# Optimization experiments

Measured on AMD Instinct MI355X. Metric: run time of the kernel, lower is better.

## Reference

```python
import jax, jax.numpy as jnp
import numpy as np

NUM_EXPERTS = 32
TOP_K = 8
HIDDEN = 1536
INTER = 512


def setup_inputs() -> dict:
    key = jax.random.key(0)
    k1, k2, k3, k4 = jax.random.split(key, 4)
    hidden_states = jax.random.normal(k1, (4, 2048, HIDDEN), dtype=jnp.float32)
    # gate (router) weight: [E, H] as in nn.Linear(hidden, num_experts)
    gate_w = jax.random.normal(k2, (NUM_EXPERTS, HIDDEN), dtype=jnp.float32) * 0.02
    # fused gate+up projection per expert: [E, 2*I, H] (first I rows = gate/silu path)
    w13 = jax.random.normal(k3, (NUM_EXPERTS, 2 * INTER, HIDDEN), dtype=jnp.float32) * 0.02
    # down projection per expert: [E, H, I]
    w2 = jax.random.normal(k4, (NUM_EXPERTS, HIDDEN, INTER), dtype=jnp.float32) * 0.02
    return {"hidden_states": hidden_states, "gate_w": gate_w, "w13": w13, "w2": w2}


def _moe_forward(x, gate_w, w13, w2):
    orig_shape = x.shape
    x = x.reshape(-1, HIDDEN)            # [T, H]
    T = x.shape[0]

    # Router: softmax over all experts, then top-k, then renormalize.
    router_logits = x @ gate_w.T          # [T, E]
    probs = jax.nn.softmax(router_logits, axis=-1)
    topk_w, topk_idx = jax.lax.top_k(probs, TOP_K)        # [T, K]
    topk_w = topk_w / jnp.sum(topk_w, axis=-1, keepdims=True)

    # Scatter top-k weights into a dense [T, E] combine matrix (zeros elsewhere).
    expert_w = jnp.zeros((T, NUM_EXPERTS), dtype=x.dtype)
    expert_w = expert_w.at[jnp.arange(T)[:, None], topk_idx].add(topk_w)
    expert_w_eT = expert_w.T              # [E, T]

    def body(acc, ew):
        we, w13_e, w2_e = ew              # [T], [2I, H], [H, I]
        gu = x @ w13_e.T                  # [T, 2I]
        g, u = gu[:, :INTER], gu[:, INTER:]
        y = (jax.nn.silu(g) * u) @ w2_e.T  # [T, H]
        return acc + we[:, None] * y, None

    out, _ = jax.lax.scan(body, jnp.zeros_like(x), (expert_w_eT, w13, w2))
    return out.reshape(orig_shape)


def reference(hidden_states, gate_w, w13, w2):
    return _moe_forward(hidden_states, gate_w, w13, w2)
```

## Files before the change

### kernel.cpp

```cpp
#include <hip/hip_runtime.h>
#include <hip/hip_bf16.h>
#include <math.h>

#define NUM_EXPERTS 32
#define TOP_K 8
#define HIDDEN 1536
#define INTER 512

typedef __bf16 bf16_t;
typedef __bf16 bf16x8 __attribute__((ext_vector_type(8)));
typedef __bf16 bf16x4 __attribute__((ext_vector_type(4)));
typedef float f32x4 __attribute__((ext_vector_type(4)));

#define M_COUNTS    0
#define M_OFFSETS   32
#define M_CURSORS   96
#define M_NUMTILES  128
#define M_TILE_E    256
#define M_TILE_M0   1024
#define M_TILE_ROWS 2048
#define META_BYTES  16384

__device__ __forceinline__ void gld16(void* lds, const void* gsrc) {
  __builtin_amdgcn_global_load_lds(
      (const __attribute__((address_space(1))) void*)gsrc,
      (__attribute__((address_space(3))) void*)lds, 16, 0, 0);
}

__global__ __launch_bounds__(256) void k_cvt(
    const float* __restrict__ src, bf16_t* __restrict__ dst)
{
  size_t i = ((size_t)blockIdx.x * 256 + threadIdx.x) * 4;
  f32x4 v = *(const f32x4*)(src + i);
  bf16x4 o;
  o[0] = (bf16_t)v[0]; o[1] = (bf16_t)v[1]; o[2] = (bf16_t)v[2]; o[3] = (bf16_t)v[3];
  *(bf16x4*)(dst + i) = o;
}

__global__ __launch_bounds__(256) void k_tgw(
    const float* __restrict__ gw, float* __restrict__ gwT4)
{
  int tid = blockIdx.x * 256 + threadIdx.x;
  int e = tid / HIDDEN, k = tid % HIDDEN;
  gwT4[(k >> 2) * 128 + (e << 2) + (k & 3)] = gw[tid];
}

__global__ __launch_bounds__(64) void k_router(
    const float* __restrict__ x, const float* __restrict__ gwT4,
    int* __restrict__ meta, int* __restrict__ topk_idx, float* __restrict__ topk_w,
    bf16_t* __restrict__ x16)
{
  int t = blockIdx.x;
  int lane = threadIdx.x;
  int e = lane & 31, part = lane >> 5;
  const float* xrow = x + (size_t)t * HIDDEN;
  const f32x4* xr = (const f32x4*)(xrow + part * 768);
  const f32x4* gr = (const f32x4*)(gwT4 + part * 192 * 128 + e * 4);
  float s = 0.f;
#pragma unroll 4
  for (int i = 0; i < 192; ++i) {
    f32x4 xv = xr[i];
    f32x4 gv = gr[i * 32];
    s += xv[0] * gv[0] + xv[1] * gv[1] + xv[2] * gv[2] + xv[3] * gv[3];
  }
  s += __shfl_xor(s, 32);

  {
    const f32x4* xv4 = (const f32x4*)(xrow + lane * 24);
    bf16_t* xo = x16 + (size_t)t * HIDDEN + lane * 24;
#pragma unroll
    for (int i = 0; i < 6; ++i) {
      f32x4 v = xv4[i];
      bf16x4 o;
      o[0] = (bf16_t)v[0]; o[1] = (bf16_t)v[1]; o[2] = (bf16_t)v[2]; o[3] = (bf16_t)v[3];
      *(bf16x4*)(xo + i * 4) = o;
    }
  }

  float logit = s, rem = s;
  float m0 = 0.f, wsum = 0.f, my_l = 0.f;
  int my_e = 0;
#pragma unroll
  for (int k = 0; k < TOP_K; ++k) {
    float mx = rem;
#pragma unroll
    for (int off = 32; off >= 1; off >>= 1) mx = fmaxf(mx, __shfl_xor(mx, off));
    unsigned long long bal = __ballot(rem == mx);
    int src = __ffsll(bal) - 1;
    int ex = src & 31;
    float lv = __shfl(logit, ex);
    if (k == 0) m0 = mx;
    wsum += __expf(lv - m0);
    if (lane == k) { my_e = ex; my_l = lv; }
    if ((lane & 31) == ex) rem = -1e30f;
  }
  if (lane < TOP_K) {
    topk_idx[t * TOP_K + lane] = my_e;
    topk_w[t * TOP_K + lane] = __expf(my_l - m0) / wsum;
    atomicAdd(&meta[M_COUNTS + my_e], 1);
  }
}

__global__ void k_scan(int* __restrict__ meta)
{
  if (threadIdx.x != 0 || blockIdx.x != 0) return;
  int off = 0, nt = 0;
  for (int e = 0; e < NUM_EXPERTS; ++e) {
    int n = meta[M_COUNTS + e];
    meta[M_OFFSETS + e] = off;
    meta[M_CURSORS + e] = off;
    int tn = (n + 127) >> 7;
    for (int i = 0; i < tn; ++i) {
      meta[M_TILE_E + nt] = e;
      meta[M_TILE_M0 + nt] = off + i * 128;
      meta[M_TILE_ROWS + nt] = min(128, n - i * 128);
      ++nt;
    }
    off += n;
  }
  meta[M_OFFSETS + NUM_EXPERTS] = off;
  meta[M_NUMTILES] = nt;
}

__global__ __launch_bounds__(256) void k_scatter(
    const int* __restrict__ topk_idx, const float* __restrict__ topk_w,
    int* __restrict__ meta, int* __restrict__ pair_token, float* __restrict__ pair_weight)
{
  int i = blockIdx.x * 256 + threadIdx.x;
  int e = topk_idx[i];
  int pos = atomicAdd(&meta[M_CURSORS + e], 1);
  pair_token[pos] = i >> 3;
  pair_weight[pos] = topk_w[i];
}

__global__ __launch_bounds__(256, 2) void k_gemm1(
    const bf16_t* __restrict__ x, const bf16_t* __restrict__ w13,
    const int* __restrict__ meta, const int* __restrict__ pair_token,
    bf16_t* __restrict__ act)
{
  int bid = blockIdx.x;
  int xcd = bid & 7, r2 = bid >> 3;
  int nb = r2 & 3, tile = xcd + 8 * (r2 >> 2);
  if (tile >= meta[M_NUMTILES]) return;
  int e    = meta[M_TILE_E + tile];
  int m0   = meta[M_TILE_M0 + tile];
  int rows = meta[M_TILE_ROWS + tile];
  int n0g  = nb * 128;

  __shared__ __align__(16) char smem[49152];
  char* As = smem;
  char* Bs = smem + 16384;

  int tid = threadIdx.x;
  int lane = tid & 63, w = tid >> 6;
  int cd = lane & 7;
  int lrow = w * 8 + (lane >> 3);

  const bf16_t* a_src[4];
  const bf16_t* b_src[8];
#pragma unroll
  for (int i = 0; i < 4; ++i) {
    int r = i * 32 + lrow;
    int rr = (r < rows) ? r : 0;
    int tok = pair_token[m0 + rr];
    int cg = cd ^ (r & 7);
    a_src[i] = x + (size_t)tok * HIDDEN + cg * 8;
  }
#pragma unroll
  for (int i = 0; i < 8; ++i) {
    int r = i * 32 + lrow;
    int cg = cd ^ (r & 7);
    int gr = (r < 128) ? (n0g + r) : (512 + n0g + (r - 128));
    b_src[i] = w13 + (size_t)e * (2 * INTER) * HIDDEN + (size_t)gr * HIDDEN + cg * 8;
  }
  unsigned lds_off = w * 1024 + lane * 16;

  f32x4 acc[2][16] = {};
  int q = lane >> 4, cl = lane & 15;
  int arow0 = (w * 32 + cl) * 128;
  int arow1 = (w * 32 + 16 + cl) * 128;

  for (int k0 = 0; k0 < HIDDEN; k0 += 64) {
#pragma unroll
    for (int i = 0; i < 4; ++i) gld16(As + i * 4096 + lds_off, a_src[i] + k0);
#pragma unroll
    for (int i = 0; i < 8; ++i) gld16(Bs + i * 4096 + lds_off, b_src[i] + k0);
    __syncthreads();
#pragma unroll
    for (int ks = 0; ks < 2; ++ks) {
      int csw = ((ks * 4 + q) ^ (lane & 7)) * 16;
      bf16x8 a0 = *(const bf16x8*)(As + arow0 + csw);
      bf16x8 a1 = *(const bf16x8*)(As + arow1 + csw);
#pragma unroll
      for (int in = 0; in < 16; ++in) {
        bf16x8 b = *(const bf16x8*)(Bs + (in * 16 + cl) * 128 + csw);
        acc[0][in] = __builtin_amdgcn_mfma_f32_16x16x32_bf16(a0, b, acc[0][in], 0, 0, 0);
        acc[1][in] = __builtin_amdgcn_mfma_f32_16x16x32_bf16(a1, b, acc[1][in], 0, 0, 0);
      }
    }
    __syncthreads();
  }

#pragma unroll
  for (int im = 0; im < 2; ++im) {
#pragma unroll
    for (int reg = 0; reg < 4; ++reg) {
      int row = w * 32 + im * 16 + q * 4 + reg;
      if (row < rows) {
        bf16_t* obase = act + (size_t)(m0 + row) * INTER + n0g + cl;
#pragma unroll
        for (int in = 0; in < 8; ++in) {
          float g = acc[im][in][reg];
          float u = acc[im][in + 8][reg];
          float a = (g / (1.f + __expf(-g))) * u;
          obase[in * 16] = (bf16_t)a;
        }
      }
    }
  }
}

__global__ __launch_bounds__(256, 2) void k_gemm2(
    const bf16_t* __restrict__ act, const bf16_t* __restrict__ w2,
    const int* __restrict__ meta, const int* __restrict__ pair_token,
    const float* __restrict__ pair_weight, float* __restrict__ out)
{
  int bid = blockIdx.x;
  int xcd = bid & 7, r2 = bid >> 3;
  int nb = r2 % 6, tile = xcd + 8 * (r2 / 6);
  if (tile >= meta[M_NUMTILES]) return;
  int e    = meta[M_TILE_E + tile];
  int m0   = meta[M_TILE_M0 + tile];
  int rows = meta[M_TILE_ROWS + tile];
  int n0   = nb * 256;

  __shared__ __align__(16) char smem[49152];
  char* As = smem;
  char* Bs = smem + 16384;

  int tid = threadIdx.x;
  int lane = tid & 63, w = tid >> 6;
  int cd = lane & 7;
  int lrow = w * 8 + (lane >> 3);

  const bf16_t* a_src[4];
  const bf16_t* b_src[8];
#pragma unroll
  for (int i = 0; i < 4; ++i) {
    int r = i * 32 + lrow;
    int rr = (r < rows) ? r : 0;
    int cg = cd ^ (r & 7);
    a_src[i] = act + (size_t)(m0 + rr) * INTER + cg * 8;
  }
#pragma unroll
  for (int i = 0; i < 8; ++i) {
    int r = i * 32 + lrow;
    int cg = cd ^ (r & 7);
    b_src[i] = w2 + (size_t)e * HIDDEN * INTER + (size_t)(n0 + r) * INTER + cg * 8;
  }
  unsigned lds_off = w * 1024 + lane * 16;

  f32x4 acc[2][16] = {};
  int q = lane >> 4, cl = lane & 15;
  int arow0 = (w * 32 + cl) * 128;
  int arow1 = (w * 32 + 16 + cl) * 128;

  for (int k0 = 0; k0 < INTER; k0 += 64) {
#pragma unroll
    for (int i = 0; i < 4; ++i) gld16(As + i * 4096 + lds_off, a_src[i] + k0);
#pragma unroll
    for (int i = 0; i < 8; ++i) gld16(Bs + i * 4096 + lds_off, b_src[i] + k0);
    __syncthreads();
#pragma unroll
    for (int ks = 0; ks < 2; ++ks) {
      int csw = ((ks * 4 + q) ^ (lane & 7)) * 16;
      bf16x8 a0 = *(const bf16x8*)(As + arow0 + csw);
      bf16x8 a1 = *(const bf16x8*)(As + arow1 + csw);
#pragma unroll
      for (int in = 0; in < 16; ++in) {
        bf16x8 b = *(const bf16x8*)(Bs + (in * 16 + cl) * 128 + csw);
        acc[0][in] = __builtin_amdgcn_mfma_f32_16x16x32_bf16(a0, b, acc[0][in], 0, 0, 0);
        acc[1][in] = __builtin_amdgcn_mfma_f32_16x16x32_bf16(a1, b, acc[1][in], 0, 0, 0);
      }
    }
    __syncthreads();
  }

#pragma unroll
  for (int im = 0; im < 2; ++im) {
#pragma unroll
    for (int reg = 0; reg < 4; ++reg) {
      int row = w * 32 + im * 16 + q * 4 + reg;
      if (row < rows) {
        int p = m0 + row;
        int tok = pair_token[p];
        float pw = pair_weight[p];
        float* obase = out + (size_t)tok * HIDDEN + n0 + cl;
#pragma unroll
        for (int in = 0; in < 16; ++in)
          unsafeAtomicAdd(obase + in * 16, acc[im][in][reg] * pw);
      }
    }
  }
}

extern "C" void kernel_launch(void* const* d_in, const int* in_sizes, int n_in,
                              void* d_out, int out_size, void* d_ws, size_t ws_size,
                              hipStream_t stream)
{
  const float* x   = (const float*)d_in[0];
  const float* gw  = (const float*)d_in[1];
  const float* w13 = (const float*)d_in[2];
  const float* w2  = (const float*)d_in[3];
  float* out = (float*)d_out;

  const int T = in_sizes[0] / HIDDEN;
  const int P = T * TOP_K;
  const size_t NX   = (size_t)T * HIDDEN;
  const size_t NW13 = (size_t)NUM_EXPERTS * 2 * INTER * HIDDEN;
  const size_t NW2  = (size_t)NUM_EXPERTS * HIDDEN * INTER;

  char* ws = (char*)d_ws;
  int*    meta        = (int*)ws;
  int*    topk_idx    = (int*)(ws + META_BYTES);
  float*  topk_w      = (float*)(ws + META_BYTES + (size_t)P * 4);
  int*    pair_token  = (int*)(ws + META_BYTES + (size_t)P * 8);
  float*  pair_weight = (float*)(ws + META_BYTES + (size_t)P * 12);
  float*  gwT4        = (float*)(ws + (1536u << 10));
  size_t off = 2u << 20;
  bf16_t* x16    = (bf16_t*)(ws + off); off += NX * 2;
  bf16_t* w13_16 = (bf16_t*)(ws + off); off += NW13 * 2;
  bf16_t* w2_16  = (bf16_t*)(ws + off); off += NW2 * 2;
  bf16_t* act    = (bf16_t*)(ws + off);

  hipMemsetAsync(meta, 0, 32 * sizeof(int), stream);
  hipMemsetAsync(out, 0, (size_t)out_size * sizeof(float), stream);

  k_tgw<<<(HIDDEN * NUM_EXPERTS) / 256, 256, 0, stream>>>(gw, gwT4);
  k_cvt<<<NW13 / 1024, 256, 0, stream>>>(w13, w13_16);
  k_cvt<<<NW2 / 1024, 256, 0, stream>>>(w2, w2_16);

  k_router<<<T, 64, 0, stream>>>(x, gwT4, meta, topk_idx, topk_w, x16);
  k_scan<<<1, 64, 0, stream>>>(meta);
  k_scatter<<<P / 256, 256, 0, stream>>>(topk_idx, topk_w, meta, pair_token, pair_weight);

  k_gemm1<<<544 * 4, 256, 0, stream>>>(x16, w13_16, meta, pair_token, act);
  k_gemm2<<<544 * 6, 256, 0, stream>>>(act, w2_16, meta, pair_token, pair_weight, out);
}
```

Measured before the change: 1.271 ms.

## Replace atomic scatter-add in down-projection with bf16 staging and gather combine

```diff
diff --git a/kernel.cpp b/kernel.cpp
--- a/kernel.cpp
+++ b/kernel.cpp
@@ -123,17 +123,17 @@
 }
 
 __global__ __launch_bounds__(256) void k_scatter(
-    const int* __restrict__ topk_idx, const float* __restrict__ topk_w,
-    int* __restrict__ meta, int* __restrict__ pair_token, float* __restrict__ pair_weight)
+    const int* __restrict__ topk_idx,
+    int* __restrict__ meta, int* __restrict__ pair_token, int* __restrict__ pair_pos)
 {
   int i = blockIdx.x * 256 + threadIdx.x;
   int e = topk_idx[i];
   int pos = atomicAdd(&meta[M_CURSORS + e], 1);
   pair_token[pos] = i >> 3;
-  pair_weight[pos] = topk_w[i];
-}
-
-__global__ __launch_bounds__(256, 2) void k_gemm1(
+  pair_pos[i] = pos;
+}
+
+__global__ __launch_bounds__(256, 3) void k_gemm1(
     const bf16_t* __restrict__ x, const bf16_t* __restrict__ w13,
     const int* __restrict__ meta, const int* __restrict__ pair_token,
     bf16_t* __restrict__ act)
@@ -220,19 +220,19 @@
   }
 }
 
-__global__ __launch_bounds__(256, 2) void k_gemm2(
+__global__ __launch_bounds__(256, 3) void k_gemm2(
     const bf16_t* __restrict__ act, const bf16_t* __restrict__ w2,
-    const int* __restrict__ meta, const int* __restrict__ pair_token,
-    const float* __restrict__ pair_weight, float* __restrict__ out)
+    const int* __restrict__ meta, bf16_t* __restrict__ y, int n0base)
 {
   int bid = blockIdx.x;
   int xcd = bid & 7, r2 = bid >> 3;
-  int nb = r2 % 6, tile = xcd + 8 * (r2 / 6);
+  int nb = r2 % 3, tile = xcd + 8 * (r2 / 3);
   if (tile >= meta[M_NUMTILES]) return;
   int e    = meta[M_TILE_E + tile];
   int m0   = meta[M_TILE_M0 + tile];
   int rows = meta[M_TILE_ROWS + tile];
-  int n0   = nb * 256;
+  int n0l  = nb * 256;
+  int n0   = n0base + n0l;
 
   __shared__ __align__(16) char smem[49152];
   char* As = smem;
@@ -292,16 +292,37 @@
     for (int reg = 0; reg < 4; ++reg) {
       int row = w * 32 + im * 16 + q * 4 + reg;
       if (row < rows) {
-        int p = m0 + row;
-        int tok = pair_token[p];
-        float pw = pair_weight[p];
-        float* obase = out + (size_t)tok * HIDDEN + n0 + cl;
+        bf16_t* obase = y + (size_t)(m0 + row) * 768 + n0l + cl;
 #pragma unroll
         for (int in = 0; in < 16; ++in)
-          unsafeAtomicAdd(obase + in * 16, acc[im][in][reg] * pw);
+          obase[in * 16] = (bf16_t)acc[im][in][reg];
       }
     }
   }
+}
+
+__global__ __launch_bounds__(256) void k_combine(
+    const bf16_t* __restrict__ y, const int* __restrict__ pair_pos,
+    const float* __restrict__ topk_w, float* __restrict__ out, int colbase)
+{
+  int idx = blockIdx.x * 256 + threadIdx.x;
+  int t = idx / 96, c = idx % 96;
+  const int*   pp = pair_pos + t * 8;
+  const float* tw = topk_w + t * 8;
+  f32x4 sa = {}, sb = {};
+#pragma unroll
+  for (int k = 0; k < 8; ++k) {
+    int pos = pp[k];
+    float wgt = tw[k];
+    bf16x8 v = *(const bf16x8*)(y + (size_t)pos * 768 + c * 8);
+    sa[0] += wgt * (float)v[0]; sa[1] += wgt * (float)v[1];
+    sa[2] += wgt * (float)v[2]; sa[3] += wgt * (float)v[3];
+    sb[0] += wgt * (float)v[4]; sb[1] += wgt * (float)v[5];
+    sb[2] += wgt * (float)v[6]; sb[3] += wgt * (float)v[7];
+  }
+  float* o = out + (size_t)t * HIDDEN + colbase + c * 8;
+  *(f32x4*)o = sa;
+  *(f32x4*)(o + 4) = sb;
 }
 
 extern "C" void kernel_launch(void* const* d_in, const int* in_sizes, int n_in,
@@ -325,16 +346,17 @@
   int*    topk_idx    = (int*)(ws + META_BYTES);
   float*  topk_w      = (float*)(ws + META_BYTES + (size_t)P * 4);
   int*    pair_token  = (int*)(ws + META_BYTES + (size_t)P * 8);
-  float*  pair_weight = (float*)(ws + META_BYTES + (size_t)P * 12);
+  int*    pair_pos    = (int*)(ws + META_BYTES + (size_t)P * 12);
   float*  gwT4        = (float*)(ws + (1536u << 10));
   size_t off = 2u << 20;
+  bf16_t* w2_16  = (bf16_t*)(ws + off); off += NW2 * 2;
+  bf16_t* act    = (bf16_t*)(ws + off); off += (size_t)P * INTER * 2;
+  size_t y_off = off;
   bf16_t* x16    = (bf16_t*)(ws + off); off += NX * 2;
-  bf16_t* w13_16 = (bf16_t*)(ws + off); off += NW13 * 2;
-  bf16_t* w2_16  = (bf16_t*)(ws + off); off += NW2 * 2;
-  bf16_t* act    = (bf16_t*)(ws + off);
+  bf16_t* w13_16 = (bf16_t*)(ws + off);
+  bf16_t* y      = (bf16_t*)(ws + y_off);
 
   hipMemsetAsync(meta, 0, 32 * sizeof(int), stream);
-  hipMemsetAsync(out, 0, (size_t)out_size * sizeof(float), stream);
 
   k_tgw<<<(HIDDEN * NUM_EXPERTS) / 256, 256, 0, stream>>>(gw, gwT4);
   k_cvt<<<NW13 / 1024, 256, 0, stream>>>(w13, w13_16);
@@ -342,8 +364,12 @@
 
   k_router<<<T, 64, 0, stream>>>(x, gwT4, meta, topk_idx, topk_w, x16);
   k_scan<<<1, 64, 0, stream>>>(meta);
-  k_scatter<<<P / 256, 256, 0, stream>>>(topk_idx, topk_w, meta, pair_token, pair_weight);
+  k_scatter<<<P / 256, 256, 0, stream>>>(topk_idx, meta, pair_token, pair_pos);
 
   k_gemm1<<<544 * 4, 256, 0, stream>>>(x16, w13_16, meta, pair_token, act);
-  k_gemm2<<<544 * 6, 256, 0, stream>>>(act, w2_16, meta, pair_token, pair_weight, out);
-}
+
+  k_gemm2<<<544 * 3, 256, 0, stream>>>(act, w2_16, meta, y, 0);
+  k_combine<<<(T * 96) / 256, 256, 0, stream>>>(y, pair_pos, topk_w, out, 0);
+  k_gemm2<<<544 * 3, 256, 0, stream>>>(act, w2_16, meta, y, 768);
+  k_combine<<<(T * 96) / 256, 256, 0, stream>>>(y, pair_pos, topk_w, out, 768);
+}
```

Result: faster. 1.195 ms (-5.9%).
